# Kernel optimization log

Measured on AMD Instinct MI355X. Metric: run time of the kernel, lower is better.

Reference implementation:

```python
import jax, jax.numpy as jnp
import numpy as np

NUM_FORMULAS = 256
NUM_CONJ_ARR = [6, 9, 12, 15]
DEPTH_ARR = [2, 4, 6]
TEMPERATURE = 2.0
INPUT_DIM = 512
BATCH = 8192

# --- static DNF structure (mirrors build-time indicator matrices) ---
_group = NUM_FORMULAS // len(NUM_CONJ_ARR)                       # 64 formulas per group
_conj_per_formula = np.repeat(np.array(NUM_CONJ_ARR), _group)     # [F]
_CONJ2FORM = np.repeat(np.arange(NUM_FORMULAS), _conj_per_formula)  # [C] = 2688
TOTAL_CONJ = int(_CONJ2FORM.shape[0])
_depths = np.tile(np.array(DEPTH_ARR), TOTAL_CONJ // len(DEPTH_ARR))  # depth per conjunction
_LIT2CONJ = np.repeat(np.arange(TOTAL_CONJ), _depths)             # [L] = 10752
TOTAL_LIT = int(_LIT2CONJ.shape[0])


def setup_inputs() -> dict:
    key = jax.random.key(0)
    k = jax.random.split(key, 6)
    x = jax.random.normal(k[0], (BATCH, INPUT_DIM), jnp.float32)
    # literals_random_mask: binary feature-subset mask per literal (build-time constant)
    random_mask = (jax.random.uniform(k[1], (INPUT_DIM, TOTAL_LIT)) < 0.5).astype(jnp.float32)
    glorot = jnp.sqrt(2.0 / (INPUT_DIM + TOTAL_LIT))
    # weight is pre-multiplied by the random mask at build time
    weight = jax.random.normal(k[2], (INPUT_DIM, TOTAL_LIT), jnp.float32) * glorot * random_mask
    # learnable_binary_mask: soft binary-threshold output in [0, 1]
    learnable_binary_mask = jax.random.uniform(k[3], (INPUT_DIM, TOTAL_LIT), jnp.float32)
    bias = jnp.zeros((TOTAL_LIT,), jnp.float32)
    mu = jax.random.normal(k[4], (NUM_FORMULAS, INPUT_DIM), jnp.float32)
    sigma = 1.0 + 0.1 * jax.random.uniform(k[5], (NUM_FORMULAS,), jnp.float32)
    return {
        "x": x, "weight": weight, "learnable_binary_mask": learnable_binary_mask,
        "bias": bias, "mu": mu, "sigma": sigma,
        "lit2conj": jnp.asarray(_LIT2CONJ, jnp.int32),
        "conj2form": jnp.asarray(_CONJ2FORM, jnp.int32),
    }


def reference(x, weight, learnable_binary_mask, bias, mu, sigma, lit2conj, conj2form):
    # literal projection: tanh(x @ (W * M) + b)             -> [B, L]
    literals = jnp.tanh(x @ (weight * learnable_binary_mask) + bias)
    # soft AND over literals of each conjunction: tanh(sum - d + 1.5)
    and_bias = jax.ops.segment_sum(jnp.ones((TOTAL_LIT,), literals.dtype), lit2conj,
                                   num_segments=TOTAL_CONJ)
    conj_sum = jax.ops.segment_sum(literals.T, lit2conj, num_segments=TOTAL_CONJ).T  # [B, C]
    conj = jnp.tanh(conj_sum - and_bias + 1.5)
    # soft OR over conjunctions of each formula: tanh(sum + d - 1.5)
    or_bias = jax.ops.segment_sum(jnp.ones((TOTAL_CONJ,), conj.dtype), conj2form,
                                  num_segments=NUM_FORMULAS)
    form_sum = jax.ops.segment_sum(conj.T, conj2form, num_segments=NUM_FORMULAS).T   # [B, F]
    dnnf = jnp.tanh(form_sum + or_bias - 1.5)
    # localization: softmax over formulas of temperature-scaled RBF, via GEMM expansion
    sq = (jnp.sum(x * x, axis=1, keepdims=True) - 2.0 * (x @ mu.T)
          + jnp.sum(mu * mu, axis=1)[None, :])                                       # [B, F]
    loc = jax.nn.softmax(TEMPERATURE * jnp.exp(-0.5 * sq / (sigma * sigma)[None, :]), axis=-1)
    return dnnf * loc
```

## Files before the change

### kernel.cpp

```cpp
#include <hip/hip_runtime.h>


#define BATCH 8192
#define IDIM 512
#define NFORM 256
#define NLIT 10752
#define WT_ROWS 11136

#define BM 256
#define BN 192
#define BK 64
#define ABYTES 32768
#define BBYTES 24576
#define BUFB 57344
#define SLITP 196

typedef __bf16 bf16x8 __attribute__((ext_vector_type(8)));
typedef float f32x4 __attribute__((ext_vector_type(4)));
typedef unsigned short u16;
typedef unsigned int u32;

__device__ __forceinline__ u16 f2bf(float f) {
  u32 u = __float_as_uint(f);
  u = (u + 0x7fffu + ((u >> 16) & 1u)) >> 16;
  return (u16)u;
}

__device__ __forceinline__ float fast_tanh(float x) {
  float e = __expf(2.0f * x);
  return 1.0f - 2.0f * __builtin_amdgcn_rcpf(e + 1.0f);
}

__device__ __forceinline__ void async_cp16(const void* g, void* l) {
  __builtin_amdgcn_global_load_lds(
      (const u32 __attribute__((address_space(1)))*)g,
      (u32 __attribute__((address_space(3)))*)l, 16, 0, 0);
}


#define PREPX_BLKS 2048
#define PREPW_BLKS 1344

__global__ __launch_bounds__(256) void prep_all(
    const float* __restrict__ x, const float* __restrict__ W,
    const float* __restrict__ M, const float* __restrict__ mu,
    u16* __restrict__ xb, u16* __restrict__ wt, float* __restrict__ xsq,
    float* __restrict__ musq, float* __restrict__ form_sum) {
  __shared__ float lds[64 * 65];
  const int blk = blockIdx.x, tid = threadIdx.x;

  if (blk < PREPX_BLKS) {
    ((uint4*)form_sum)[blk * 256 + tid] = make_uint4(0, 0, 0, 0);
    int wave = tid >> 6, lane = tid & 63;
    int row = blk * 4 + wave;
    const float4* px = (const float4*)(x + (size_t)row * IDIM);
    float4 a = px[lane * 2], b = px[lane * 2 + 1];
    uint4 pk;
    pk.x = (u32)f2bf(a.x) | ((u32)f2bf(a.y) << 16);
    pk.y = (u32)f2bf(a.z) | ((u32)f2bf(a.w) << 16);
    pk.z = (u32)f2bf(b.x) | ((u32)f2bf(b.y) << 16);
    pk.w = (u32)f2bf(b.z) | ((u32)f2bf(b.w) << 16);
    ((uint4*)(xb + (size_t)row * IDIM))[lane] = pk;
    float s = a.x * a.x + a.y * a.y + a.z * a.z + a.w * a.w +
              b.x * b.x + b.y * b.y + b.z * b.z + b.w * b.w;
#pragma unroll
    for (int o = 32; o > 0; o >>= 1) s += __shfl_down(s, o);
    if (lane == 0) xsq[row] = s;
  } else if (blk < PREPX_BLKS + PREPW_BLKS) {
    int b = blk - PREPX_BLKS;
    int l0 = (b % 168) * 64, k0 = (b / 168) * 64;
#pragma unroll
    for (int j = 0; j < 4; ++j) {
      int idx = tid + j * 256;
      int kk = idx >> 4, l4 = idx & 15;
      size_t g = (size_t)(k0 + kk) * NLIT + l0 + l4 * 4;
      float4 w4 = *(const float4*)(W + g);
      float4 m4 = *(const float4*)(M + g);
      lds[kk * 65 + l4 * 4 + 0] = w4.x * m4.x;
      lds[kk * 65 + l4 * 4 + 1] = w4.y * m4.y;
      lds[kk * 65 + l4 * 4 + 2] = w4.z * m4.z;
      lds[kk * 65 + l4 * 4 + 3] = w4.w * m4.w;
    }
    __syncthreads();
    int l = tid >> 2, kq = tid & 3;
    u32 pk[8];
#pragma unroll
    for (int t = 0; t < 8; ++t) {
      u16 lo = f2bf(lds[(kq * 16 + 2 * t) * 65 + l]);
      u16 hi = f2bf(lds[(kq * 16 + 2 * t + 1) * 65 + l]);
      pk[t] = (u32)lo | ((u32)hi << 16);
    }
    u32* dst = (u32*)(wt + (size_t)(l0 + l) * IDIM + k0 + kq * 16);
    ((uint4*)dst)[0] = make_uint4(pk[0], pk[1], pk[2], pk[3]);
    ((uint4*)dst)[1] = make_uint4(pk[4], pk[5], pk[6], pk[7]);
  } else {
    int b = blk - PREPX_BLKS - PREPW_BLKS;
    if (b < 256) {
      float s = 0.f;
#pragma unroll
      for (int j = tid; j < IDIM; j += 256) {
        float v = mu[(size_t)b * IDIM + j];
        wt[(size_t)(NLIT + b) * IDIM + j] = f2bf(v);
        s += v * v;
      }
      float* red = lds;
      red[tid] = s;
      __syncthreads();
      for (int sh = 128; sh > 0; sh >>= 1) {
        if (tid < sh) red[tid] += red[tid + sh];
        __syncthreads();
      }
      if (tid == 0) musq[b] = red[0];
    } else {
      int row = NLIT + 256 + (b - 256);
      for (int j = tid; j < IDIM; j += 256) wt[(size_t)row * IDIM + j] = 0;
    }
  }
}


__global__ __launch_bounds__(512, 2) void dnnf_gemm(
    const u16* __restrict__ xb, const u16* __restrict__ wt,
    const float* __restrict__ bias, float* __restrict__ form_sum,
    float* __restrict__ dotbuf) {
  __shared__ __align__(16) char smraw[2 * BUFB];
  float* slit = (float*)smraw;

  const int tid = threadIdx.x;
  const int wave = tid >> 6, lane = tid & 63;
  const int wm = wave & 3, wn = wave >> 2;
  const int m0 = blockIdx.x * BM, n0 = blockIdx.y * BN;
  const int q = lane >> 4, cn = lane & 15;

  const int kg8 = ((tid & 7) ^ ((tid >> 3) & 7)) * 8;
  const u16* pa = xb + (size_t)(m0 + (tid >> 3)) * IDIM + kg8;
  const u16* pb = wt + (size_t)(n0 + (tid >> 3)) * IDIM + kg8;
  const int dA = tid * 16;
  const int dB = ABYTES + tid * 16;

  const int kg0_16 = ((q ^ (cn & 7)) << 4);
  int offA[4], offB[6];
#pragma unroll
  for (int mf = 0; mf < 4; ++mf)
    offA[mf] = (wm * 64 + mf * 16 + cn) * 128 + kg0_16;
#pragma unroll
  for (int nf = 0; nf < 6; ++nf)
    offB[nf] = ABYTES + (wn * 96 + nf * 16 + cn) * 128 + kg0_16;

  f32x4 acc[4][6];
#pragma unroll
  for (int a = 0; a < 4; ++a)
#pragma unroll
    for (int b = 0; b < 6; ++b) acc[a][b] = (f32x4){0.f, 0.f, 0.f, 0.f};

#pragma unroll
  for (int i = 0; i < 4; ++i)
    async_cp16(pa + (size_t)i * 64 * IDIM, smraw + dA + i * 8192);
#pragma unroll
  for (int i = 0; i < 3; ++i)
    async_cp16(pb + (size_t)i * 64 * IDIM, smraw + dB + i * 8192);
  pa += BK;
  pb += BK;

#pragma unroll
  for (int kt = 0; kt < 8; ++kt) {
    const char* bufc = smraw + (kt & 1) * BUFB;
    if (kt < 7) {
      char* bufn = smraw + ((kt + 1) & 1) * BUFB;
#pragma unroll
      for (int i = 0; i < 4; ++i)
        async_cp16(pa + (size_t)i * 64 * IDIM, bufn + dA + i * 8192);
#pragma unroll
      for (int i = 0; i < 3; ++i)
        async_cp16(pb + (size_t)i * 64 * IDIM, bufn + dB + i * 8192);
      pa += BK;
      pb += BK;
      asm volatile("s_waitcnt vmcnt(7)\n\ts_barrier" ::: "memory");
    } else {
      asm volatile("s_waitcnt vmcnt(0)\n\ts_barrier" ::: "memory");
    }
#pragma unroll
    for (int ks = 0; ks < 2; ++ks) {
      const int x64 = ks ? 64 : 0;
      bf16x8 af[4], bfr[6];
#pragma unroll
      for (int mf = 0; mf < 4; ++mf)
        af[mf] = *(const bf16x8*)(bufc + (offA[mf] ^ x64));
#pragma unroll
      for (int nf = 0; nf < 6; ++nf)
        bfr[nf] = *(const bf16x8*)(bufc + (offB[nf] ^ x64));
#pragma unroll
      for (int mf = 0; mf < 4; ++mf)
#pragma unroll
        for (int nf = 0; nf < 6; ++nf)
          acc[mf][nf] = __builtin_amdgcn_mfma_f32_16x16x32_bf16(
              af[mf], bfr[nf], acc[mf][nf], 0, 0, 0);
    }
    if (kt < 7)
      asm volatile("s_waitcnt lgkmcnt(0)\n\ts_barrier" ::: "memory");
  }
  __syncthreads();

  if (n0 < NLIT) {
    float bv[6];
#pragma unroll
    for (int nf = 0; nf < 6; ++nf) bv[nf] = bias[n0 + wn * 96 + nf * 16 + cn];

#pragma unroll
    for (int ph = 0; ph < 2; ++ph) {
      if (ph) __syncthreads();
      if ((wm >> 1) == ph) {
#pragma unroll
        for (int nf = 0; nf < 6; ++nf) {
          int col = wn * 96 + nf * 16 + cn;
#pragma unroll
          for (int mf = 0; mf < 4; ++mf)
#pragma unroll
            for (int reg = 0; reg < 4; ++reg) {
              int lr = (wm & 1) * 64 + mf * 16 + q * 4 + reg;
              slit[lr * SLITP + col] = fast_tanh(acc[mf][nf][reg] + bv[nf]);
            }
        }
      }
      __syncthreads();

      int r = tid >> 2, sub = tid & 3;
      const float* lrow = slit + r * SLITP + sub * 48;
      int c0 = ((n0 + sub * 48) / 12) * 3;
      size_t grow = (size_t)(m0 + ph * 128 + r) * NFORM;
      float run = 0.f;
      int fprev = -1;
#pragma unroll
      for (int tr = 0; tr < 4; ++tr) {
        const float* p = lrow + tr * 12;
        float s2 = p[0] + p[1];
        float s4 = p[2] + p[3] + p[4] + p[5];
        float s6 = p[6] + p[7] + p[8] + p[9] + p[10] + p[11];
        float v = fast_tanh(s2 - 0.5f) + fast_tanh(s4 - 2.5f) +
                  fast_tanh(s6 - 4.5f);
        int c = c0 + tr * 3;
        int f = (c < 384)    ? (c / 6)
                : (c < 960)  ? 64 + (c - 384) / 9
                : (c < 1728) ? 128 + (c - 960) / 12
                             : 192 + (c - 1728) / 15;
        if (f != fprev) {
          if (fprev >= 0) atomicAdd(form_sum + grow + fprev, run);
          fprev = f;
          run = 0.f;
        }
        run += v;
      }
      atomicAdd(form_sum + grow + fprev, run);
    }
  } else {
#pragma unroll
    for (int nf = 0; nf < 6; ++nf) {
      int col = n0 - NLIT + wn * 96 + nf * 16 + cn;
      if (col < NFORM) {
#pragma unroll
        for (int mf = 0; mf < 4; ++mf)
#pragma unroll
          for (int reg = 0; reg < 4; ++reg) {
            int row = wm * 64 + mf * 16 + q * 4 + reg;
            dotbuf[(size_t)(m0 + row) * NFORM + col] = acc[mf][nf][reg];
          }
      }
    }
  }
}


__global__ __launch_bounds__(256) void finale(
    const float* __restrict__ form_sum, const float* __restrict__ dotbuf,
    const float* __restrict__ xsq, const float* __restrict__ musq,
    const float* __restrict__ sigma, float* __restrict__ out) {
  int wave = threadIdx.x >> 6, lane = threadIdx.x & 63;
  int r = blockIdx.x * 4 + wave;
  size_t base = (size_t)r * NFORM;
  float xs = xsq[r];
  float e[4], s = 0.f;
#pragma unroll
  for (int j = 0; j < 4; ++j) {
    int f = j * 64 + lane;
    float sq = xs - 2.0f * dotbuf[base + f] + musq[f];
    float sg = sigma[f];
    float p = __expf(-0.5f * sq / (sg * sg));
    e[j] = __expf(2.0f * p);
    s += e[j];
  }
#pragma unroll
  for (int o = 32; o > 0; o >>= 1) s += __shfl_xor(s, o);
  float inv = __builtin_amdgcn_rcpf(s);
#pragma unroll
  for (int j = 0; j < 4; ++j) {
    int f = j * 64 + lane;
    float dn = fast_tanh(form_sum[base + f] + (float)(6 + 3 * j) - 1.5f);
    out[base + f] = dn * e[j] * inv;
  }
}


extern "C" void kernel_launch(void* const* d_in, const int* in_sizes, int n_in,
                              void* d_out, int out_size, void* d_ws,
                              size_t ws_size, hipStream_t stream) {
  const float* x = (const float*)d_in[0];
  const float* W = (const float*)d_in[1];
  const float* M = (const float*)d_in[2];
  const float* bias = (const float*)d_in[3];
  const float* mu = (const float*)d_in[4];
  const float* sigma = (const float*)d_in[5];
  float* out = (float*)d_out;

  float* form_sum = (float*)d_ws;
  float* dotbuf = form_sum + (size_t)BATCH * NFORM;
  u16* xb = (u16*)(dotbuf + (size_t)BATCH * NFORM);
  u16* wt = xb + (size_t)BATCH * IDIM;
  float* xsq = (float*)(wt + (size_t)WT_ROWS * IDIM);
  float* musq = xsq + BATCH;

  prep_all<<<PREPX_BLKS + PREPW_BLKS + 384, 256, 0, stream>>>(
      x, W, M, mu, xb, wt, xsq, musq, form_sum);
  dnnf_gemm<<<dim3(BATCH / BM, WT_ROWS / BN), 512, 0, stream>>>(xb, wt, bias,
                                                                form_sum, dotbuf);
  finale<<<BATCH / 4, 256, 0, stream>>>(form_sum, dotbuf, xsq, musq, sigma, out);
}
```

Baseline: 270.2 us.

## Restructure GEMM main loop into interleaved staged loads with 2x4 wave layout

Changes the wave tiling from 4x2 (64x96 per wave) to 2x4 (128x48 per wave) and rewrites the K loop as a fine-grained schedule. Each sub-phase interleaves LDS fragment reads, partial async global-to-LDS copies for the next tile, and MFMA groups raised with s_setprio. The goal is to hide LDS and global latency behind MFMA work and cut barrier stalls. It adds many more barriers and more register pressure from the double-k fragments. The epilogue also switches to float4 LDS reads for the conjunction sums.

```diff
diff --git a/kernel.cpp b/kernel.cpp
--- a/kernel.cpp
+++ b/kernel.cpp
@@ -10,9 +10,7 @@
 #define BM 256
 #define BN 192
 #define BK 64
-#define ABYTES 32768
-#define BBYTES 24576
-#define BUFB 57344
+#define TBUF 57344
 #define SLITP 196
 
 typedef __bf16 bf16x8 __attribute__((ext_vector_type(8)));
@@ -123,119 +121,171 @@
     const u16* __restrict__ xb, const u16* __restrict__ wt,
     const float* __restrict__ bias, float* __restrict__ form_sum,
     float* __restrict__ dotbuf) {
-  __shared__ __align__(16) char smraw[2 * BUFB];
+  __shared__ __align__(16) char smraw[2 * TBUF];
   float* slit = (float*)smraw;
 
   const int tid = threadIdx.x;
   const int wave = tid >> 6, lane = tid & 63;
-  const int wm = wave & 3, wn = wave >> 2;
+  const int wm = wave >> 2, wn = wave & 3;
   const int m0 = blockIdx.x * BM, n0 = blockIdx.y * BN;
   const int q = lane >> 4, cn = lane & 15;
 
-  const int kg8 = ((tid & 7) ^ ((tid >> 3) & 7)) * 8;
-  const u16* pa = xb + (size_t)(m0 + (tid >> 3)) * IDIM + kg8;
-  const u16* pb = wt + (size_t)(n0 + (tid >> 3)) * IDIM + kg8;
-  const int dA = tid * 16;
-  const int dB = ABYTES + tid * 16;
-
-  const int kg0_16 = ((q ^ (cn & 7)) << 4);
-  int offA[4], offB[6];
-#pragma unroll
-  for (int mf = 0; mf < 4; ++mf)
-    offA[mf] = (wm * 64 + mf * 16 + cn) * 128 + kg0_16;
-#pragma unroll
-  for (int nf = 0; nf < 6; ++nf)
-    offB[nf] = ABYTES + (wn * 96 + nf * 16 + cn) * 128 + kg0_16;
-
-  f32x4 acc[4][6];
-#pragma unroll
-  for (int a = 0; a < 4; ++a)
-#pragma unroll
-    for (int b = 0; b < 6; ++b) acc[a][b] = (f32x4){0.f, 0.f, 0.f, 0.f};
-
-#pragma unroll
-  for (int i = 0; i < 4; ++i)
-    async_cp16(pa + (size_t)i * 64 * IDIM, smraw + dA + i * 8192);
-#pragma unroll
-  for (int i = 0; i < 3; ++i)
-    async_cp16(pb + (size_t)i * 64 * IDIM, smraw + dB + i * 8192);
-  pa += BK;
-  pb += BK;
-
-#pragma unroll
-  for (int kt = 0; kt < 8; ++kt) {
-    const char* bufc = smraw + (kt & 1) * BUFB;
-    if (kt < 7) {
-      char* bufn = smraw + ((kt + 1) & 1) * BUFB;
-#pragma unroll
-      for (int i = 0; i < 4; ++i)
-        async_cp16(pa + (size_t)i * 64 * IDIM, bufn + dA + i * 8192);
-#pragma unroll
-      for (int i = 0; i < 3; ++i)
-        async_cp16(pb + (size_t)i * 64 * IDIM, bufn + dB + i * 8192);
-      pa += BK;
-      pb += BK;
-      asm volatile("s_waitcnt vmcnt(7)\n\ts_barrier" ::: "memory");
-    } else {
-      asm volatile("s_waitcnt vmcnt(0)\n\ts_barrier" ::: "memory");
-    }
-#pragma unroll
-    for (int ks = 0; ks < 2; ++ks) {
-      const int x64 = ks ? 64 : 0;
-      bf16x8 af[4], bfr[6];
-#pragma unroll
-      for (int mf = 0; mf < 4; ++mf)
-        af[mf] = *(const bf16x8*)(bufc + (offA[mf] ^ x64));
-#pragma unroll
-      for (int nf = 0; nf < 6; ++nf)
-        bfr[nf] = *(const bf16x8*)(bufc + (offB[nf] ^ x64));
-#pragma unroll
-      for (int mf = 0; mf < 4; ++mf)
-#pragma unroll
-        for (int nf = 0; nf < 6; ++nf)
-          acc[mf][nf] = __builtin_amdgcn_mfma_f32_16x16x32_bf16(
-              af[mf], bfr[nf], acc[mf][nf], 0, 0, 0);
-    }
-    if (kt < 7)
-      asm volatile("s_waitcnt lgkmcnt(0)\n\ts_barrier" ::: "memory");
+  const int sr = tid >> 3;
+  const int kgs = ((tid & 7) ^ (sr & 7)) * 8;
+  const u16* pa = xb + (size_t)(m0 + sr) * IDIM + kgs;
+  const u16* pb = wt + (size_t)(n0 + sr) * IDIM + kgs;
+  const int ldsd = tid * 16;
+
+  const int swz = (q ^ (cn & 7)) << 4;
+  int offA[8], offB[3];
+#pragma unroll
+  for (int mf = 0; mf < 8; ++mf)
+    offA[mf] = (wm * 128 + mf * 16 + cn) * 128 + swz;
+#pragma unroll
+  for (int nf = 0; nf < 3; ++nf)
+    offB[nf] = 32768 + (wn * 48 + nf * 16 + cn) * 128 + swz;
+
+  f32x4 acc[8][3];
+#pragma unroll
+  for (int a = 0; a < 8; ++a)
+#pragma unroll
+    for (int b = 0; b < 3; ++b) acc[a][b] = (f32x4){0.f, 0.f, 0.f, 0.f};
+
+  bf16x8 af[4][2], bfr[3][2];
+
+#define STG_A(bi, u, t)                                  \
+  async_cp16(pa + (size_t)(u) * 64 * IDIM + (t) * BK,    \
+             smraw + (bi) * TBUF + (u) * 8192 + ldsd)
+#define STG_B(bi, u, t)                                  \
+  async_cp16(pb + (size_t)(u) * 64 * IDIM + (t) * BK,    \
+             smraw + (bi) * TBUF + 32768 + (u) * 8192 + ldsd)
+#define RD_A(bi, msh)                                               \
+  do {                                                              \
+    const char* bp_ = smraw + (bi) * TBUF;                          \
+    _Pragma("unroll") for (int i_ = 0; i_ < 4; ++i_) {              \
+      af[i_][0] = *(const bf16x8*)(bp_ + offA[(msh) * 4 + i_]);     \
+      af[i_][1] = *(const bf16x8*)(bp_ + (offA[(msh) * 4 + i_] ^ 64)); \
+    }                                                               \
+  } while (0)
+#define RD_B01(bi)                                                  \
+  do {                                                              \
+    const char* bp_ = smraw + (bi) * TBUF;                          \
+    _Pragma("unroll") for (int j_ = 0; j_ < 2; ++j_) {              \
+      bfr[j_][0] = *(const bf16x8*)(bp_ + offB[j_]);                \
+      bfr[j_][1] = *(const bf16x8*)(bp_ + (offB[j_] ^ 64));         \
+    }                                                               \
+  } while (0)
+#define RD_B2(bi)                                                   \
+  do {                                                              \
+    const char* bp_ = smraw + (bi) * TBUF;                          \
+    bfr[2][0] = *(const bf16x8*)(bp_ + offB[2]);                    \
+    bfr[2][1] = *(const bf16x8*)(bp_ + (offB[2] ^ 64));             \
+  } while (0)
+#define MM(msh, nflo, nfhi)                                         \
+  do {                                                              \
+    __builtin_amdgcn_s_setprio(1);                                  \
+    _Pragma("unroll") for (int i_ = 0; i_ < 4; ++i_)                \
+    _Pragma("unroll") for (int n_ = (nflo); n_ <= (nfhi); ++n_)     \
+    _Pragma("unroll") for (int k_ = 0; k_ < 2; ++k_)                \
+      acc[(msh) * 4 + i_][n_] = __builtin_amdgcn_mfma_f32_16x16x32_bf16( \
+          af[i_][k_], bfr[n_][k_], acc[(msh) * 4 + i_][n_], 0, 0, 0);    \
+    __builtin_amdgcn_s_setprio(0);                                  \
+  } while (0)
+#define BAR asm volatile("s_barrier" ::: "memory")
+#define BARV asm volatile("s_waitcnt vmcnt(7)\n\ts_barrier" ::: "memory")
+#define BARL asm volatile("s_waitcnt lgkmcnt(0)\n\ts_barrier" ::: "memory")
+
+#pragma unroll
+  for (int u = 0; u < 4; ++u) STG_A(0, u, 0);
+#pragma unroll
+  for (int u = 0; u < 3; ++u) STG_B(0, u, 0);
+#pragma unroll
+  for (int u = 0; u < 4; ++u) STG_A(1, u, 1);
+#pragma unroll
+  for (int u = 0; u < 3; ++u) STG_B(1, u, 1);
+  BARV;
+
+#pragma unroll
+  for (int it = 0; it < 4; ++it) {
+    const int s0 = 2 * it + 2, s1 = 2 * it + 3;
+    RD_A(0, 0);
+    RD_B01(0);
+    BAR;
+    MM(0, 0, 1);
+    BARL;
+    RD_B2(0);
+    if (it < 3) { STG_A(0, 0, s0); STG_A(0, 2, s0); }
+    BAR;
+    MM(0, 2, 2);
+    BARL;
+    RD_A(0, 1);
+    if (it < 3) { STG_B(0, 0, s0); STG_B(0, 1, s0); STG_B(0, 2, s0); }
+    BAR;
+    MM(1, 0, 1);
+    BARL;
+    if (it < 3) { STG_A(0, 1, s0); STG_A(0, 3, s0); }
+    BARV;
+    MM(1, 2, 2);
+    BAR;
+    RD_A(1, 0);
+    RD_B01(1);
+    BAR;
+    MM(0, 0, 1);
+    BARL;
+    RD_B2(1);
+    if (it < 3) { STG_A(1, 0, s1); STG_A(1, 2, s1); }
+    BAR;
+    MM(0, 2, 2);
+    BARL;
+    RD_A(1, 1);
+    if (it < 3) { STG_B(1, 0, s1); STG_B(1, 1, s1); STG_B(1, 2, s1); }
+    BAR;
+    MM(1, 0, 1);
+    BARL;
+    if (it < 3) { STG_A(1, 1, s1); STG_A(1, 3, s1); }
+    BARV;
+    MM(1, 2, 2);
+    BAR;
   }
   __syncthreads();
 
   if (n0 < NLIT) {
-    float bv[6];
-#pragma unroll
-    for (int nf = 0; nf < 6; ++nf) bv[nf] = bias[n0 + wn * 96 + nf * 16 + cn];
+    float bv[3];
+#pragma unroll
+    for (int nf = 0; nf < 3; ++nf) bv[nf] = bias[n0 + wn * 48 + nf * 16 + cn];
 
 #pragma unroll
     for (int ph = 0; ph < 2; ++ph) {
       if (ph) __syncthreads();
-      if ((wm >> 1) == ph) {
-#pragma unroll
-        for (int nf = 0; nf < 6; ++nf) {
-          int col = wn * 96 + nf * 16 + cn;
-#pragma unroll
-          for (int mf = 0; mf < 4; ++mf)
+      if (wm == ph) {
+#pragma unroll
+        for (int nf = 0; nf < 3; ++nf) {
+          int col = wn * 48 + nf * 16 + cn;
+#pragma unroll
+          for (int mf = 0; mf < 8; ++mf)
 #pragma unroll
             for (int reg = 0; reg < 4; ++reg) {
-              int lr = (wm & 1) * 64 + mf * 16 + q * 4 + reg;
+              int lr = mf * 16 + q * 4 + reg;
               slit[lr * SLITP + col] = fast_tanh(acc[mf][nf][reg] + bv[nf]);
             }
         }
       }
       __syncthreads();
 
-      int r = tid >> 2, sub = tid & 3;
-      const float* lrow = slit + r * SLITP + sub * 48;
+      int rr = tid >> 2, sub = tid & 3;
+      const float* lrow = slit + rr * SLITP + sub * 48;
       int c0 = ((n0 + sub * 48) / 12) * 3;
-      size_t grow = (size_t)(m0 + ph * 128 + r) * NFORM;
+      size_t grow = (size_t)(m0 + ph * 128 + rr) * NFORM;
       float run = 0.f;
       int fprev = -1;
 #pragma unroll
       for (int tr = 0; tr < 4; ++tr) {
-        const float* p = lrow + tr * 12;
-        float s2 = p[0] + p[1];
-        float s4 = p[2] + p[3] + p[4] + p[5];
-        float s6 = p[6] + p[7] + p[8] + p[9] + p[10] + p[11];
+        const float4 a0 = *(const float4*)(lrow + tr * 12);
+        const float4 a1 = *(const float4*)(lrow + tr * 12 + 4);
+        const float4 a2 = *(const float4*)(lrow + tr * 12 + 8);
+        float s2 = a0.x + a0.y;
+        float s4 = a0.z + a0.w + a1.x + a1.y;
+        float s6 = a1.z + a1.w + a2.x + a2.y + a2.z + a2.w;
         float v = fast_tanh(s2 - 0.5f) + fast_tanh(s4 - 2.5f) +
                   fast_tanh(s6 - 4.5f);
         int c = c0 + tr * 3;
@@ -254,14 +304,14 @@
     }
   } else {
 #pragma unroll
-    for (int nf = 0; nf < 6; ++nf) {
-      int col = n0 - NLIT + wn * 96 + nf * 16 + cn;
+    for (int nf = 0; nf < 3; ++nf) {
+      int col = n0 - NLIT + wn * 48 + nf * 16 + cn;
       if (col < NFORM) {
 #pragma unroll
-        for (int mf = 0; mf < 4; ++mf)
+        for (int mf = 0; mf < 8; ++mf)
 #pragma unroll
           for (int reg = 0; reg < 4; ++reg) {
-            int row = wm * 64 + mf * 16 + q * 4 + reg;
+            int row = wm * 128 + mf * 16 + q * 4 + reg;
             dotbuf[(size_t)(m0 + row) * NFORM + col] = acc[mf][nf][reg];
           }
       }
```

Result: faster. 262.6 us (-2.8%).
